# Performance work log

Hardware: AMD Instinct MI355X
Metric: run time of the kernel (lower is better)

Reference implementation:

```python
import jax, jax.numpy as jnp
import numpy as np

B, H, G, N, D = 1, 32, 64, 128, 128   # batch, heads, blocks, block_len, head_dim
S = 256                               # sketch dim (multiple of 16)
BIT_PACK = 8


def setup_inputs() -> dict:
    key = jax.random.key(0)
    k1, k2, k3 = jax.random.split(key, 3)
    data = jax.random.normal(k1, (B, H, G, N, D), dtype=jnp.float32)
    # binary per-channel outlier mask, float {0,1}, shape matches data.shape[:3] + (D,)
    outlier_mask = jax.random.randint(k2, (B, H, G, D), 0, 2).astype(jnp.float32)
    # proj_dir_quant = proj_dir_score.T -> shape (S, D)
    proj_dir_quant = jax.random.normal(k3, (S, D), dtype=jnp.float32)
    return {"data": data, "outlier_mask": outlier_mask, "proj_dir_quant": proj_dir_quant}


def _pack_bits(sketch):
    # sketch: (..., S). Reshape to (..., S//8, 8), threshold at 0, pack sign bits into uint8.
    x = sketch.reshape(*sketch.shape[:-1], -1, BIT_PACK)
    enc = (2 ** jnp.arange(BIT_PACK, dtype=jnp.int32))  # [1,2,4,...,128]
    packed = ((x > 0).astype(jnp.int32) * enc).sum(axis=-1)  # max 255, fits uint8
    return packed.astype(jnp.uint8)


def reference(data, outlier_mask, proj_dir_quant):
    s = proj_dir_quant.shape[0]
    m = outlier_mask[..., None, :]                     # (B,H,G,1,D) broadcast over tokens
    key_outlier = data * m
    key_inlier = data * (1.0 - m)
    # '...nd,sd->...ns' : sign-random-projection sketch
    sk_outlier = jnp.einsum('bhgnd,sd->bhgns', key_outlier, proj_dir_quant)
    sk_inlier = jnp.einsum('bhgnd,sd->bhgns', key_inlier, proj_dir_quant)
    hash_inlier = _pack_bits(sk_inlier)                # (B,H,G,N,S//8)
    hash_outlier = _pack_bits(sk_outlier)[..., : s // 16]  # (B,H,G,N,S//16)
    return (hash_inlier, hash_outlier)
```

## Files before the change

kernel.cpp:

```cpp
#include <hip/hip_runtime.h>

#define NB_HG 2048
#define DIM_N 128
#define DIM_D 128
#define DIM_S 256


__global__ void transpose_proj_kernel(const float* __restrict__ proj,
                                      float* __restrict__ projT)
{
    const int d = blockIdx.x;
    const int s = threadIdx.x;
    projT[d * DIM_S + s] = proj[s * DIM_D + d];
}

template<bool TP>
__global__ __launch_bounds__(256)
void qjl_sketch_kernel(const float* __restrict__ data,
                       const float* __restrict__ mask,
                       const float* __restrict__ pmat,
                       int* __restrict__ out)
{
    __shared__ float Xt[DIM_D * DIM_N];
    __shared__ int   din[DIM_D];
    __shared__ int   dout[DIM_D];
    __shared__ int   win[2];

    const int hg  = blockIdx.x;
    const int tid = threadIdx.x;

    const int  lane = tid & 63;
    const int  w    = tid >> 6;
    bool is_in = false; int rank_in = 0;
    if (tid < 128) {
        const float m = mask[hg * DIM_D + tid];
        is_in = (m == 0.0f);
        const unsigned long long bal = __ballot(is_in);
        if (lane == 0) win[w] = __popcll(bal);
        rank_in = __popcll(bal & ((1ull << lane) - 1ull));
    }
    __syncthreads();
    const int Kin = win[0] + win[1];
    if (tid < 128) {
        if (is_in) din [rank_in          + (w ? win[0]        : 0)] = tid;
        else       dout[(lane - rank_in) + (w ? (64 - win[0]) : 0)] = tid;
    }

    {
        const int d  = tid & 127;
        const int nh = tid >> 7;
        const float* Xs = data + (size_t)hg * (DIM_N * DIM_D) + d;
        const int pcs = 4 * (d & 7);
        float* row = &Xt[d * DIM_N];
        #pragma unroll
        for (int g = 0; g < 16; ++g) {
            const int n0 = g * 8 + nh * 4;
            float4 v;
            v.x = Xs[(size_t)(n0 + 0) * DIM_D];
            v.y = Xs[(size_t)(n0 + 1) * DIM_D];
            v.z = Xs[(size_t)(n0 + 2) * DIM_D];
            v.w = Xs[(size_t)(n0 + 3) * DIM_D];
            *reinterpret_cast<float4*>(&row[n0 ^ pcs]) = v;
        }
    }
    __syncthreads();

    const int tn = tid & 15;
    const int ts = tid >> 4;
    const int C0 = 4 * tn;
    const int sl = ts * 8;
    const size_t inl_total = (size_t)NB_HG * DIM_N * 32;

    auto PASS = [&](const int* __restrict__ list, int cnt, int sbase, int typ) {
        float acc[8][8];
        #pragma unroll
        for (int j = 0; j < 8; ++j)
            #pragma unroll
            for (int i = 0; i < 8; ++i) acc[j][i] = 0.0f;

        #pragma unroll 4
        for (int ci = 0; ci < cnt; ++ci) {
            const int dl = list[ci];
            float4 b0, b1;
            if (TP) {
                const float* pr = pmat + (size_t)dl * DIM_S + sbase + sl;
                b0 = *reinterpret_cast<const float4*>(pr);
                b1 = *reinterpret_cast<const float4*>(pr + 4);
            } else {
                b0.x = pmat[(size_t)(sbase + sl + 0) * DIM_D + dl];
                b0.y = pmat[(size_t)(sbase + sl + 1) * DIM_D + dl];
                b0.z = pmat[(size_t)(sbase + sl + 2) * DIM_D + dl];
                b0.w = pmat[(size_t)(sbase + sl + 3) * DIM_D + dl];
                b1.x = pmat[(size_t)(sbase + sl + 4) * DIM_D + dl];
                b1.y = pmat[(size_t)(sbase + sl + 5) * DIM_D + dl];
                b1.z = pmat[(size_t)(sbase + sl + 6) * DIM_D + dl];
                b1.w = pmat[(size_t)(sbase + sl + 7) * DIM_D + dl];
            }
            const int pcs = 4 * (dl & 7);
            const int P   = C0 ^ pcs;
            const float* r = &Xt[dl * DIM_N + P];
            const float4 q0 = *reinterpret_cast<const float4*>(r);
            const float4 q1 = *reinterpret_cast<const float4*>(r + 64);
            const float bv[8] = {b0.x, b0.y, b0.z, b0.w, b1.x, b1.y, b1.z, b1.w};

            #pragma unroll
            for (int j = 0; j < 8; ++j) {
                acc[j][0] = fmaf(bv[j], q0.x, acc[j][0]);
                acc[j][1] = fmaf(bv[j], q0.y, acc[j][1]);
                acc[j][2] = fmaf(bv[j], q0.z, acc[j][2]);
                acc[j][3] = fmaf(bv[j], q0.w, acc[j][3]);
                acc[j][4] = fmaf(bv[j], q1.x, acc[j][4]);
                acc[j][5] = fmaf(bv[j], q1.y, acc[j][5]);
                acc[j][6] = fmaf(bv[j], q1.z, acc[j][6]);
                acc[j][7] = fmaf(bv[j], q1.w, acc[j][7]);
            }
        }

        #pragma unroll
        for (int i = 0; i < 8; ++i) {
            int byte = 0;
            #pragma unroll
            for (int j = 0; j < 8; ++j)
                if (acc[j][i] > 0.0f) byte |= (1 << j);
            const int n = (i < 4) ? (C0 + i) : (64 + C0 + (i - 4));
            size_t idx;
            if (typ == 2)
                idx = inl_total + ((size_t)hg * DIM_N + n) * 16 + ts;
            else
                idx = ((size_t)hg * DIM_N + n) * 32 + (typ == 1 ? 16 : 0) + ts;
            out[idx] = byte;
        }
    };

    PASS(din,  Kin,         0,   0);
    PASS(din,  Kin,         128, 1);
    PASS(dout, DIM_D - Kin, 0,   2);

}

extern "C" void kernel_launch(void* const* d_in, const int* in_sizes, int n_in,
                              void* d_out, int out_size, void* d_ws, size_t ws_size,
                              hipStream_t stream) {
    const float* data = (const float*)d_in[0];
    const float* mask = (const float*)d_in[1];
    const float* proj = (const float*)d_in[2];
    int* out = (int*)d_out;

    const size_t tp_bytes = (size_t)DIM_D * DIM_S * sizeof(float);
    if (ws_size >= tp_bytes) {
        float* projT = (float*)d_ws;
        transpose_proj_kernel<<<DIM_D, DIM_S, 0, stream>>>(proj, projT);
        qjl_sketch_kernel<true><<<NB_HG, 256, 0, stream>>>(data, mask, projT, out);
    } else {
        qjl_sketch_kernel<false><<<NB_HG, 256, 0, stream>>>(data, mask, proj, out);
    }
}
```

Baseline: 191.3 us.

## Merge inlier sketch halves into one pass with 16x8 register tile per thread

The two inlier passes over the S=0..127 and S=128..255 halves become one pass in which each thread accumulates 16 sketch columns by 8 tokens. Each LDS read of X is now reused across twice as many projection columns, and the din list and X rows are walked only once. The outlier pass is remapped to 32 token groups by 8 sketch groups with a 16x4 tile. Launch bounds now request 2 blocks per CU, which limits registers while the accumulator array grows to 128 floats, so spilling or lower occupancy is a risk.

```diff
diff --git a/kernel.cpp b/kernel.cpp
--- a/kernel.cpp
+++ b/kernel.cpp
@@ -15,7 +15,7 @@
 }
 
 template<bool TP>
-__global__ __launch_bounds__(256)
+__global__ __launch_bounds__(256, 2)
 void qjl_sketch_kernel(const float* __restrict__ data,
                        const float* __restrict__ mask,
                        const float* __restrict__ pmat,
@@ -65,46 +65,48 @@
     }
     __syncthreads();
 
-    const int tn = tid & 15;
-    const int ts = tid >> 4;
-    const int C0 = 4 * tn;
-    const int sl = ts * 8;
     const size_t inl_total = (size_t)NB_HG * DIM_N * 32;
-
-    auto PASS = [&](const int* __restrict__ list, int cnt, int sbase, int typ) {
-        float acc[8][8];
-        #pragma unroll
-        for (int j = 0; j < 8; ++j)
+    const size_t orow = (size_t)hg * DIM_N;
+
+    {
+        const int tn = tid & 15;
+        const int ts = tid >> 4;
+        const int C0 = 4 * tn;
+        const int sb = 16 * ts;
+
+        float acc[16][8];
+        #pragma unroll
+        for (int j = 0; j < 16; ++j)
             #pragma unroll
             for (int i = 0; i < 8; ++i) acc[j][i] = 0.0f;
 
-        #pragma unroll 4
-        for (int ci = 0; ci < cnt; ++ci) {
-            const int dl = list[ci];
-            float4 b0, b1;
+        #pragma unroll 2
+        for (int ci = 0; ci < Kin; ++ci) {
+            const int dl = din[ci];
+            float bv[16];
             if (TP) {
-                const float* pr = pmat + (size_t)dl * DIM_S + sbase + sl;
-                b0 = *reinterpret_cast<const float4*>(pr);
-                b1 = *reinterpret_cast<const float4*>(pr + 4);
+                const float* pr = pmat + (size_t)dl * DIM_S + sb;
+                const float4 b0 = *reinterpret_cast<const float4*>(pr);
+                const float4 b1 = *reinterpret_cast<const float4*>(pr + 4);
+                const float4 b2 = *reinterpret_cast<const float4*>(pr + 8);
+                const float4 b3 = *reinterpret_cast<const float4*>(pr + 12);
+                bv[0]=b0.x; bv[1]=b0.y; bv[2]=b0.z; bv[3]=b0.w;
+                bv[4]=b1.x; bv[5]=b1.y; bv[6]=b1.z; bv[7]=b1.w;
+                bv[8]=b2.x; bv[9]=b2.y; bv[10]=b2.z; bv[11]=b2.w;
+                bv[12]=b3.x; bv[13]=b3.y; bv[14]=b3.z; bv[15]=b3.w;
             } else {
-                b0.x = pmat[(size_t)(sbase + sl + 0) * DIM_D + dl];
-                b0.y = pmat[(size_t)(sbase + sl + 1) * DIM_D + dl];
-                b0.z = pmat[(size_t)(sbase + sl + 2) * DIM_D + dl];
-                b0.w = pmat[(size_t)(sbase + sl + 3) * DIM_D + dl];
-                b1.x = pmat[(size_t)(sbase + sl + 4) * DIM_D + dl];
-                b1.y = pmat[(size_t)(sbase + sl + 5) * DIM_D + dl];
-                b1.z = pmat[(size_t)(sbase + sl + 6) * DIM_D + dl];
-                b1.w = pmat[(size_t)(sbase + sl + 7) * DIM_D + dl];
+                #pragma unroll
+                for (int jj = 0; jj < 16; ++jj)
+                    bv[jj] = pmat[(size_t)(sb + jj) * DIM_D + dl];
             }
             const int pcs = 4 * (dl & 7);
             const int P   = C0 ^ pcs;
             const float* r = &Xt[dl * DIM_N + P];
             const float4 q0 = *reinterpret_cast<const float4*>(r);
             const float4 q1 = *reinterpret_cast<const float4*>(r + 64);
-            const float bv[8] = {b0.x, b0.y, b0.z, b0.w, b1.x, b1.y, b1.z, b1.w};
-
-            #pragma unroll
-            for (int j = 0; j < 8; ++j) {
+
+            #pragma unroll
+            for (int j = 0; j < 16; ++j) {
                 acc[j][0] = fmaf(bv[j], q0.x, acc[j][0]);
                 acc[j][1] = fmaf(bv[j], q0.y, acc[j][1]);
                 acc[j][2] = fmaf(bv[j], q0.z, acc[j][2]);
@@ -118,24 +120,78 @@
 
         #pragma unroll
         for (int i = 0; i < 8; ++i) {
-            int byte = 0;
-            #pragma unroll
-            for (int j = 0; j < 8; ++j)
-                if (acc[j][i] > 0.0f) byte |= (1 << j);
+            int b0 = 0, b1 = 0;
+            #pragma unroll
+            for (int j = 0; j < 8; ++j) {
+                if (acc[j][i]     > 0.0f) b0 |= (1 << j);
+                if (acc[j + 8][i] > 0.0f) b1 |= (1 << j);
+            }
             const int n = (i < 4) ? (C0 + i) : (64 + C0 + (i - 4));
-            size_t idx;
-            if (typ == 2)
-                idx = inl_total + ((size_t)hg * DIM_N + n) * 16 + ts;
-            else
-                idx = ((size_t)hg * DIM_N + n) * 32 + (typ == 1 ? 16 : 0) + ts;
-            out[idx] = byte;
-        }
-    };
-
-    PASS(din,  Kin,         0,   0);
-    PASS(din,  Kin,         128, 1);
-    PASS(dout, DIM_D - Kin, 0,   2);
-
+            const size_t base = (orow + n) * 32 + 2 * ts;
+            out[base]     = b0;
+            out[base + 1] = b1;
+        }
+    }
+
+    {
+        const int Kout = DIM_D - Kin;
+        const int tn2 = tid & 31;
+        const int ts2 = tid >> 5;
+        const int C0o = 4 * tn2;
+        const int sb2 = 16 * ts2;
+
+        float acc[16][4];
+        #pragma unroll
+        for (int j = 0; j < 16; ++j)
+            #pragma unroll
+            for (int i = 0; i < 4; ++i) acc[j][i] = 0.0f;
+
+        #pragma unroll 2
+        for (int ci = 0; ci < Kout; ++ci) {
+            const int dl = dout[ci];
+            float bv[16];
+            if (TP) {
+                const float* pr = pmat + (size_t)dl * DIM_S + sb2;
+                const float4 b0 = *reinterpret_cast<const float4*>(pr);
+                const float4 b1 = *reinterpret_cast<const float4*>(pr + 4);
+                const float4 b2 = *reinterpret_cast<const float4*>(pr + 8);
+                const float4 b3 = *reinterpret_cast<const float4*>(pr + 12);
+                bv[0]=b0.x; bv[1]=b0.y; bv[2]=b0.z; bv[3]=b0.w;
+                bv[4]=b1.x; bv[5]=b1.y; bv[6]=b1.z; bv[7]=b1.w;
+                bv[8]=b2.x; bv[9]=b2.y; bv[10]=b2.z; bv[11]=b2.w;
+                bv[12]=b3.x; bv[13]=b3.y; bv[14]=b3.z; bv[15]=b3.w;
+            } else {
+                #pragma unroll
+                for (int jj = 0; jj < 16; ++jj)
+                    bv[jj] = pmat[(size_t)(sb2 + jj) * DIM_D + dl];
+            }
+            const int pcs = 4 * (dl & 7);
+            const int P   = C0o ^ pcs;
+            const float4 q0 = *reinterpret_cast<const float4*>(&Xt[dl * DIM_N + P]);
+
+            #pragma unroll
+            for (int j = 0; j < 16; ++j) {
+                acc[j][0] = fmaf(bv[j], q0.x, acc[j][0]);
+                acc[j][1] = fmaf(bv[j], q0.y, acc[j][1]);
+                acc[j][2] = fmaf(bv[j], q0.z, acc[j][2]);
+                acc[j][3] = fmaf(bv[j], q0.w, acc[j][3]);
+            }
+        }
+
+        #pragma unroll
+        for (int i = 0; i < 4; ++i) {
+            int b0 = 0, b1 = 0;
+            #pragma unroll
+            for (int j = 0; j < 8; ++j) {
+                if (acc[j][i]     > 0.0f) b0 |= (1 << j);
+                if (acc[j + 8][i] > 0.0f) b1 |= (1 << j);
+            }
+            const int n = C0o + i;
+            const size_t base = inl_total + (orow + n) * 16 + 2 * ts2;
+            out[base]     = b0;
+            out[base + 1] = b1;
+        }
+    }
 }
 
 extern "C" void kernel_launch(void* const* d_in, const int* in_sizes, int n_in,
```

Result: slower. 195.4 us (+2.1%).

## Remap threads so each wave shares a wave-uniform projection slice loaded as scalars

Applied to the files above, without the earlier changes.

Changes the thread-to-output mapping. Each wave now owns a 32-wide slice of sketch dimensions, and each lane owns two token rows. The projection row index is forced wave-uniform with readfirstlane, so projection values can come through scalar loads instead of per-lane vector loads. LDS traffic per lane also drops to one float2 per channel. The cost is 64 accumulators per thread, which raises register pressure, and output stores become four consecutive ints per token row at a lane stride.

```diff
diff --git a/kernel.cpp b/kernel.cpp
--- a/kernel.cpp
+++ b/kernel.cpp
@@ -28,22 +28,22 @@
 
     const int hg  = blockIdx.x;
     const int tid = threadIdx.x;
+    const int l   = tid & 63;
+    const int w   = tid >> 6;
 
-    const int  lane = tid & 63;
-    const int  w    = tid >> 6;
     bool is_in = false; int rank_in = 0;
     if (tid < 128) {
         const float m = mask[hg * DIM_D + tid];
         is_in = (m == 0.0f);
         const unsigned long long bal = __ballot(is_in);
-        if (lane == 0) win[w] = __popcll(bal);
-        rank_in = __popcll(bal & ((1ull << lane) - 1ull));
+        if (l == 0) win[w] = __popcll(bal);
+        rank_in = __popcll(bal & ((1ull << l) - 1ull));
     }
     __syncthreads();
     const int Kin = win[0] + win[1];
     if (tid < 128) {
-        if (is_in) din [rank_in          + (w ? win[0]        : 0)] = tid;
-        else       dout[(lane - rank_in) + (w ? (64 - win[0]) : 0)] = tid;
+        if (is_in) din [rank_in       + (w ? win[0]        : 0)] = tid;
+        else       dout[(l - rank_in) + (w ? (64 - win[0]) : 0)] = tid;
     }
 
     {
@@ -65,77 +65,60 @@
     }
     __syncthreads();
 
-    const int tn = tid & 15;
-    const int ts = tid >> 4;
-    const int C0 = 4 * tn;
-    const int sl = ts * 8;
     const size_t inl_total = (size_t)NB_HG * DIM_N * 32;
+    const size_t orow = (size_t)hg * DIM_N;
+    const int chunk = l >> 1;
+    const int sub2  = 2 * (l & 1);
 
-    auto PASS = [&](const int* __restrict__ list, int cnt, int sbase, int typ) {
-        float acc[8][8];
+    auto PASS = [&](const int* __restrict__ list, int cnt, int swin,
+                    size_t obase, int obytes_per_n) {
+        float acc[32][2];
         #pragma unroll
-        for (int j = 0; j < 8; ++j)
-            #pragma unroll
-            for (int i = 0; i < 8; ++i) acc[j][i] = 0.0f;
+        for (int j = 0; j < 32; ++j) { acc[j][0] = 0.0f; acc[j][1] = 0.0f; }
 
-        #pragma unroll 4
+        #pragma unroll 2
         for (int ci = 0; ci < cnt; ++ci) {
-            const int dl = list[ci];
-            float4 b0, b1;
+            const int dl  = list[ci];
+            const int sdg = __builtin_amdgcn_readfirstlane(dl);
+
+            float b[32];
             if (TP) {
-                const float* pr = pmat + (size_t)dl * DIM_S + sbase + sl;
-                b0 = *reinterpret_cast<const float4*>(pr);
-                b1 = *reinterpret_cast<const float4*>(pr + 4);
+                const float* pr = pmat + (size_t)sdg * DIM_S + swin;
+                #pragma unroll
+                for (int j = 0; j < 32; ++j) b[j] = pr[j];
             } else {
-                b0.x = pmat[(size_t)(sbase + sl + 0) * DIM_D + dl];
-                b0.y = pmat[(size_t)(sbase + sl + 1) * DIM_D + dl];
-                b0.z = pmat[(size_t)(sbase + sl + 2) * DIM_D + dl];
-                b0.w = pmat[(size_t)(sbase + sl + 3) * DIM_D + dl];
-                b1.x = pmat[(size_t)(sbase + sl + 4) * DIM_D + dl];
-                b1.y = pmat[(size_t)(sbase + sl + 5) * DIM_D + dl];
-                b1.z = pmat[(size_t)(sbase + sl + 6) * DIM_D + dl];
-                b1.w = pmat[(size_t)(sbase + sl + 7) * DIM_D + dl];
+                #pragma unroll
+                for (int j = 0; j < 32; ++j)
+                    b[j] = pmat[(size_t)(swin + j) * DIM_D + sdg];
             }
-            const int pcs = 4 * (dl & 7);
-            const int P   = C0 ^ pcs;
-            const float* r = &Xt[dl * DIM_N + P];
-            const float4 q0 = *reinterpret_cast<const float4*>(r);
-            const float4 q1 = *reinterpret_cast<const float4*>(r + 64);
-            const float bv[8] = {b0.x, b0.y, b0.z, b0.w, b1.x, b1.y, b1.z, b1.w};
+
+            const int phys = ((chunk ^ (dl & 7)) << 2) + sub2;
+            const float2 q = *reinterpret_cast<const float2*>(&Xt[dl * DIM_N + phys]);
 
             #pragma unroll
-            for (int j = 0; j < 8; ++j) {
-                acc[j][0] = fmaf(bv[j], q0.x, acc[j][0]);
-                acc[j][1] = fmaf(bv[j], q0.y, acc[j][1]);
-                acc[j][2] = fmaf(bv[j], q0.z, acc[j][2]);
-                acc[j][3] = fmaf(bv[j], q0.w, acc[j][3]);
-                acc[j][4] = fmaf(bv[j], q1.x, acc[j][4]);
-                acc[j][5] = fmaf(bv[j], q1.y, acc[j][5]);
-                acc[j][6] = fmaf(bv[j], q1.z, acc[j][6]);
-                acc[j][7] = fmaf(bv[j], q1.w, acc[j][7]);
+            for (int j = 0; j < 32; ++j) {
+                acc[j][0] = fmaf(b[j], q.x, acc[j][0]);
+                acc[j][1] = fmaf(b[j], q.y, acc[j][1]);
             }
         }
 
         #pragma unroll
-        for (int i = 0; i < 8; ++i) {
-            int byte = 0;
+        for (int i = 0; i < 2; ++i) {
+            const int n = 2 * l + i;
             #pragma unroll
-            for (int j = 0; j < 8; ++j)
-                if (acc[j][i] > 0.0f) byte |= (1 << j);
-            const int n = (i < 4) ? (C0 + i) : (64 + C0 + (i - 4));
-            size_t idx;
-            if (typ == 2)
-                idx = inl_total + ((size_t)hg * DIM_N + n) * 16 + ts;
-            else
-                idx = ((size_t)hg * DIM_N + n) * 32 + (typ == 1 ? 16 : 0) + ts;
-            out[idx] = byte;
+            for (int byte = 0; byte < 4; ++byte) {
+                int v = 0;
+                #pragma unroll
+                for (int bit = 0; bit < 8; ++bit)
+                    if (acc[byte * 8 + bit][i] > 0.0f) v |= (1 << bit);
+                out[obase + (size_t)n * obytes_per_n + (swin >> 3) + byte] = v;
+            }
         }
     };
 
-    PASS(din,  Kin,         0,   0);
-    PASS(din,  Kin,         128, 1);
-    PASS(dout, DIM_D - Kin, 0,   2);
-
+    PASS(din,  Kin,          w * 32,       orow * 32,             32);
+    PASS(din,  Kin,          128 + w * 32, orow * 32,             32);
+    PASS(dout, DIM_D - Kin,  w * 32,       inl_total + orow * 16, 16);
 }
 
 extern "C" void kernel_launch(void* const* d_in, const int* in_sizes, int n_in,
```

Result: slower. 379.0 us (+98.1%).
